# Optimization experiments

Hardware: AMD Instinct MI355X
Metric: run time of the kernel (lower is better)

Reference implementation:

```python
import jax, jax.numpy as jnp
import numpy as np

KS = 2
K = 3 * KS**2 + 3 * KS + 1  # 19 hex-stencil sites
MUL = 16                     # multiplicity of each irrep block
C0 = 0.28209479177387814     # Y_0 integral-normalized, 1/(2*sqrt(pi))
C1 = 0.4886025119029199      # Y_1 coeff, sqrt(3/(4*pi))


def _hex_offsets(ks):
    """Hexagonal stencil offsets in the exact order of spin2coltri2d (center first)."""
    hexagon = [[1, 1], [1, 0], [0, -1], [-1, -1], [-1, 0], [0, 1]]
    offs = [(0, 0)]
    for k in range(1, ks + 1):
        for l in range(6 * k):
            eb = hexagon[l // k]
            ea = hexagon[(l // k + 1) % 6]
            offs.append((eb[0] * (k - l % k) + ea[0] * (l % k),
                         eb[1] * (k - l % k) + ea[1] * (l % k)))
    return offs  # length K


def setup_inputs() -> dict:
    key = jax.random.key(0)
    k1, k2, k3, k4, k5, k6, k7 = jax.random.split(key, 7)
    N, Lx, Ly = 4, 128, 128
    feat = jax.random.normal(k1, (N, Lx, Ly, 4 * MUL), dtype=jnp.float32)
    spin = jax.random.normal(k2, (N, Lx, Ly, 3), dtype=jnp.float32)
    # 'uvw' TensorProduct weights: one (mul_in, mul_out) block per hex position per path
    wshape = (K, MUL, MUL)
    w000 = jax.random.normal(k3, wshape, dtype=jnp.float32)  # 0e x 0e -> 0e
    w011 = jax.random.normal(k4, wshape, dtype=jnp.float32)  # 0e x 1e -> 1e
    w101 = jax.random.normal(k5, wshape, dtype=jnp.float32)  # 1e x 0e -> 1e
    w110 = jax.random.normal(k6, wshape, dtype=jnp.float32)  # 1e x 1e -> 0e (dot)
    w111 = jax.random.normal(k7, wshape, dtype=jnp.float32)  # 1e x 1e -> 1e (cross)
    return {"feat": feat, "spin": spin, "w000": w000, "w011": w011,
            "w101": w101, "w110": w110, "w111": w111}


def reference(feat, spin, w000, w011, w101, w110, w111):
    # --- spin2coltri2d: circular hex-stencil gather via rolls (no pad copy) ---
    offs = _hex_offsets(KS)
    col = jnp.stack([jnp.roll(feat, shift=(-ox, -oy), axis=(1, 2))
                     for (ox, oy) in offs], axis=3)  # (N,Lx,Ly,K,64)
    s = col[..., :MUL]                                       # scalars (N,Lx,Ly,K,16)
    v = col[..., MUL:].reshape(col.shape[:4] + (MUL, 3))     # vectors (N,Lx,Ly,K,16,3)
    # --- spherical harmonics of spin, l=0..1, normalize=False, integral norm ---
    sh1 = C1 * spin[..., jnp.array([1, 2, 0])]               # e3nn l=1 order (y,z,x)
    # --- CG tensor product, path-normalized per output irrep ---
    a_s = 1.0 / np.sqrt(2 * K * MUL)   # two paths feed scalar out
    a_v = 1.0 / np.sqrt(3 * K * MUL)   # three paths feed vector out
    out_s = C0 * jnp.einsum('nxyku,kuw->nxyw', s, w000)
    out_s = out_s + jnp.einsum('nxykui,nxyi,kuw->nxyw', v, sh1, w110) / np.sqrt(3.0)
    out_s = a_s * out_s
    out_v = jnp.einsum('nxyku,nxyi,kuw->nxywi', s, sh1, w011)
    out_v = out_v + C0 * jnp.einsum('nxykui,kuw->nxywi', v, w101)
    cross = jnp.cross(v, sh1[:, :, :, None, None, :])        # 1e x 1e -> 1e
    out_v = out_v + jnp.einsum('nxykui,kuw->nxywi', cross, w111) / np.sqrt(2.0)
    out_v = a_v * out_v
    return jnp.concatenate(
        [out_s, out_v.reshape(out_v.shape[:3] + (3 * MUL,))], axis=-1)
```

## Files before the change

kernel.cpp:

```cpp
#include <hip/hip_runtime.h>

typedef __attribute__((ext_vector_type(8))) short short8;
typedef __attribute__((ext_vector_type(4))) float f32x4;
typedef __attribute__((ext_vector_type(4))) int i32x4;

#define C0F 0.28209479177387814f
#define C1F 0.4886025119029199f
#define IS3 0.5773502691896258f
#define IS2 0.7071067811865476f
#define ASC 0.040555354f
#define AVC 0.033113308f

#define WB 51200
#define FB 30720
#define LDS_TOTAL (WB + FB)

__constant__ int c_doff[20] = {0, 21,20,-1,-21,-20,1,
                               42,41,40,19,-2,-22,-42,-41,-40,-19,2,22, 0};

__device__ inline unsigned short f32_bf16(float x) {
    unsigned int u = __float_as_uint(x);
    return (unsigned short)((u + 0x7FFF + ((u >> 16) & 1)) >> 16);
}

#define GLD16(gp, lp) __builtin_amdgcn_global_load_lds( \
    (const __attribute__((address_space(1))) unsigned int*)(gp), \
    (__attribute__((address_space(3))) unsigned int*)(lp), 16, 0, 0)

__global__ __launch_bounds__(256) void prep_kernel(
    const float* __restrict__ feat,
    const float* __restrict__ w000, const float* __restrict__ w011,
    const float* __restrict__ w101, const float* __restrict__ w110,
    const float* __restrict__ w111, unsigned char* __restrict__ ws)
{
    const int t = threadIdx.x;
    if (blockIdx.x >= 2048) {
        int o = (blockIdx.x - 2048) * 256 + t;
        int m = o / 5120;
        int r1 = o - m * 5120;
        int tap = r1 >> 8;
        int r2 = r1 & 255;
        int w = r2 >> 4;
        int u = r2 & 15;
        const float* W = (m == 0) ? w000 : (m == 1) ? w011 : (m == 2) ? w101 : (m == 3) ? w110 : w111;
        float val = (tap < 19) ? W[tap * 256 + u * 16 + w] : 0.0f;
        ((unsigned short*)ws)[o] = f32_bf16(val);
        return;
    }
    __shared__ float raw[2048];
    const int P0 = blockIdx.x * 32;
    const float4* src = (const float4*)feat + (size_t)P0 * 16;
    float4 l0 = src[t * 2];
    float4 l1 = src[t * 2 + 1];
    *(float4*)&raw[t * 8] = l0;
    *(float4*)&raw[t * 8 + 4] = l1;
    __syncthreads();
    const int p = t >> 3;
    const int c = t & 7;
    const float* r = &raw[p * 64];
    int ch0, stride;
    if (c < 2) { ch0 = c * 8; stride = 1; }
    else { int i = (c - 2) >> 1, uh = (c - 2) & 1; ch0 = 16 + i + 24 * uh; stride = 3; }
    unsigned int pk[4];
#pragma unroll
    for (int e = 0; e < 4; ++e) {
        unsigned int lo = f32_bf16(r[ch0 + stride * (2 * e)]);
        unsigned int hi = f32_bf16(r[ch0 + stride * (2 * e + 1)]);
        pk[e] = lo | (hi << 16);
    }
    const int PX = P0 + p;
    const int gy = PX & 127, gx = (PX >> 7) & 127;
    const int k = (4 * gx + gy + 2) & 7;
    *(i32x4*)(ws + WB + (size_t)PX * 128 + ((c ^ k) << 4)) = *(const i32x4*)pk;
}

__global__ __launch_bounds__(256) void spinconv_mfma(
    const unsigned char* __restrict__ ws, const float* __restrict__ spin,
    float* __restrict__ out)
{
    extern __shared__ char smem[];
    const int tid = threadIdx.x, b = blockIdx.x;
    const int n = b >> 7;
    const int X0 = ((b >> 3) & 15) << 3;
    const int Y0 = (b & 7) << 4;
    const int lane = tid & 63, wv = tid >> 6;
    const int lx = lane & 15;
    const int q = lane >> 4;

    float sp[24];
#pragma unroll
    for (int ti = 0; ti < 2; ++ti)
#pragma unroll
        for (int r = 0; r < 4; ++r) {
            const int x = X0 + 2 * wv + ti;
            const int y = Y0 + (q << 2) + r;
            const int P = (((n << 7) + x) << 7) + y;
            sp[ti * 12 + r * 3 + 0] = spin[3 * P + 0];
            sp[ti * 12 + r * 3 + 1] = spin[3 * P + 1];
            sp[ti * 12 + r * 3 + 2] = spin[3 * P + 2];
        }

    for (int j = 0; j < 13; ++j) {
        const int cid = j * 4 + wv;
        if (cid < 50)
            GLD16(ws + cid * 1024 + lane * 16, smem + cid * 1024);
    }
    const unsigned char* fsrc = ws + WB;
    for (int j = 0; j < 8; ++j) {
        const int cid = j * 4 + wv;
        if (cid < 30) {
            const int sl = cid * 8 + (lane >> 3);
            const int cc = lane & 7;
            const int dx = sl / 20, dy = sl - dx * 20;
            const int gx = (X0 - 2 + dx) & 127;
            const int gy = (Y0 - 2 + dy) & 127;
            GLD16(fsrc + (size_t)((((n << 7) + gx) << 7) + gy) * 128 + cc * 16,
                  smem + WB + cid * 1024);
        }
    }
    __syncthreads();

    const int u0b = (q & 1) << 4;
    const int taph = q >> 1;
    const char* flds = smem + WB;
    const int s0a = (2 * wv + 2) * 20 + lx + 2;
    const int s0b = s0a + 20;

    f32x4 aS0{0,0,0,0}, aS1{0,0,0,0}, aB0{0,0,0,0}, aB1{0,0,0,0}, aB2{0,0,0,0},
          aC0{0,0,0,0}, aC1{0,0,0,0}, aC2{0,0,0,0}, aD0{0,0,0,0}, aD1{0,0,0,0}, aD2{0,0,0,0};
    f32x4 bS0{0,0,0,0}, bS1{0,0,0,0}, bB0{0,0,0,0}, bB1{0,0,0,0}, bB2{0,0,0,0},
          bC0{0,0,0,0}, bC1{0,0,0,0}, bC2{0,0,0,0}, bD0{0,0,0,0}, bD1{0,0,0,0}, bD2{0,0,0,0};

#pragma unroll
    for (int t = 0; t < 10; ++t) {
        const int tap = 2 * t + taph;
        const int d = c_doff[tap];
        const int stA = s0a + d;
        const char* pa = flds + stA * 128;
        const int ka = (stA & 7) << 4;
        short8 xs  = *(const short8*)(pa + ((u0b      ) ^ ka));
        short8 x0  = *(const short8*)(pa + ((u0b + 32) ^ ka));
        short8 x1  = *(const short8*)(pa + ((u0b + 64) ^ ka));
        short8 x2  = *(const short8*)(pa + ((u0b + 96) ^ ka));
        const int stB = s0b + d;
        const char* pb = flds + stB * 128;
        const int kb = (stB & 7) << 4;
        short8 ys  = *(const short8*)(pb + ((u0b      ) ^ kb));
        short8 y0  = *(const short8*)(pb + ((u0b + 32) ^ kb));
        short8 y1  = *(const short8*)(pb + ((u0b + 64) ^ kb));
        short8 y2  = *(const short8*)(pb + ((u0b + 96) ^ kb));
        const char* bb = smem + tap * 512 + lx * 32 + u0b;
        short8 b000 = *(const short8*)(bb);
        short8 b011 = *(const short8*)(bb + 10240);
        short8 b101 = *(const short8*)(bb + 20480);
        short8 b110 = *(const short8*)(bb + 30720);
        short8 b111 = *(const short8*)(bb + 40960);
        aS0 = __builtin_amdgcn_mfma_f32_16x16x32_bf16(xs, b000, aS0, 0, 0, 0);
        aS1 = __builtin_amdgcn_mfma_f32_16x16x32_bf16(xs, b011, aS1, 0, 0, 0);
        aB0 = __builtin_amdgcn_mfma_f32_16x16x32_bf16(x0, b101, aB0, 0, 0, 0);
        aC0 = __builtin_amdgcn_mfma_f32_16x16x32_bf16(x0, b110, aC0, 0, 0, 0);
        aD0 = __builtin_amdgcn_mfma_f32_16x16x32_bf16(x0, b111, aD0, 0, 0, 0);
        aB1 = __builtin_amdgcn_mfma_f32_16x16x32_bf16(x1, b101, aB1, 0, 0, 0);
        aC1 = __builtin_amdgcn_mfma_f32_16x16x32_bf16(x1, b110, aC1, 0, 0, 0);
        aD1 = __builtin_amdgcn_mfma_f32_16x16x32_bf16(x1, b111, aD1, 0, 0, 0);
        aB2 = __builtin_amdgcn_mfma_f32_16x16x32_bf16(x2, b101, aB2, 0, 0, 0);
        aC2 = __builtin_amdgcn_mfma_f32_16x16x32_bf16(x2, b110, aC2, 0, 0, 0);
        aD2 = __builtin_amdgcn_mfma_f32_16x16x32_bf16(x2, b111, aD2, 0, 0, 0);
        bS0 = __builtin_amdgcn_mfma_f32_16x16x32_bf16(ys, b000, bS0, 0, 0, 0);
        bS1 = __builtin_amdgcn_mfma_f32_16x16x32_bf16(ys, b011, bS1, 0, 0, 0);
        bB0 = __builtin_amdgcn_mfma_f32_16x16x32_bf16(y0, b101, bB0, 0, 0, 0);
        bC0 = __builtin_amdgcn_mfma_f32_16x16x32_bf16(y0, b110, bC0, 0, 0, 0);
        bD0 = __builtin_amdgcn_mfma_f32_16x16x32_bf16(y0, b111, bD0, 0, 0, 0);
        bB1 = __builtin_amdgcn_mfma_f32_16x16x32_bf16(y1, b101, bB1, 0, 0, 0);
        bC1 = __builtin_amdgcn_mfma_f32_16x16x32_bf16(y1, b110, bC1, 0, 0, 0);
        bD1 = __builtin_amdgcn_mfma_f32_16x16x32_bf16(y1, b111, bD1, 0, 0, 0);
        bB2 = __builtin_amdgcn_mfma_f32_16x16x32_bf16(y2, b101, bB2, 0, 0, 0);
        bC2 = __builtin_amdgcn_mfma_f32_16x16x32_bf16(y2, b110, bC2, 0, 0, 0);
        bD2 = __builtin_amdgcn_mfma_f32_16x16x32_bf16(y2, b111, bD2, 0, 0, 0);
    }

    const int w = lx;
#pragma unroll
    for (int r = 0; r < 4; ++r) {
        const int y = Y0 + (q << 2) + r;
        {
            const int x = X0 + 2 * wv;
            const int P = (((n << 7) + x) << 7) + y;
            const float s0 = C1F * sp[r * 3 + 1];
            const float s1 = C1F * sp[r * 3 + 2];
            const float s2 = C1F * sp[r * 3 + 0];
            float* o = out + (size_t)P * 64;
            o[w] = ASC * (C0F * aS0[r] + IS3 * (s0 * aC0[r] + s1 * aC1[r] + s2 * aC2[r]));
            o[16 + 3 * w + 0] = AVC * (s0 * aS1[r] + C0F * aB0[r] + IS2 * (s2 * aD1[r] - s1 * aD2[r]));
            o[16 + 3 * w + 1] = AVC * (s1 * aS1[r] + C0F * aB1[r] + IS2 * (s0 * aD2[r] - s2 * aD0[r]));
            o[16 + 3 * w + 2] = AVC * (s2 * aS1[r] + C0F * aB2[r] + IS2 * (s1 * aD0[r] - s0 * aD1[r]));
        }
        {
            const int x = X0 + 2 * wv + 1;
            const int P = (((n << 7) + x) << 7) + y;
            const float s0 = C1F * sp[12 + r * 3 + 1];
            const float s1 = C1F * sp[12 + r * 3 + 2];
            const float s2 = C1F * sp[12 + r * 3 + 0];
            float* o = out + (size_t)P * 64;
            o[w] = ASC * (C0F * bS0[r] + IS3 * (s0 * bC0[r] + s1 * bC1[r] + s2 * bC2[r]));
            o[16 + 3 * w + 0] = AVC * (s0 * bS1[r] + C0F * bB0[r] + IS2 * (s2 * bD1[r] - s1 * bD2[r]));
            o[16 + 3 * w + 1] = AVC * (s1 * bS1[r] + C0F * bB1[r] + IS2 * (s0 * bD2[r] - s2 * bD0[r]));
            o[16 + 3 * w + 2] = AVC * (s2 * bS1[r] + C0F * bB2[r] + IS2 * (s1 * bD0[r] - s0 * bD1[r]));
        }
    }
}

extern "C" void kernel_launch(void* const* d_in, const int* in_sizes, int n_in,
                              void* d_out, int out_size, void* d_ws, size_t ws_size,
                              hipStream_t stream) {
    const float* feat = (const float*)d_in[0];
    const float* spin = (const float*)d_in[1];
    const float* w000 = (const float*)d_in[2];
    const float* w011 = (const float*)d_in[3];
    const float* w101 = (const float*)d_in[4];
    const float* w110 = (const float*)d_in[5];
    const float* w111 = (const float*)d_in[6];
    float* out = (float*)d_out;
    unsigned char* ws = (unsigned char*)d_ws;

    static bool attr_set = false;
    if (!attr_set) {
        (void)hipFuncSetAttribute((const void*)spinconv_mfma,
                                  hipFuncAttributeMaxDynamicSharedMemorySize, LDS_TOTAL);
        attr_set = true;
    }

    hipLaunchKernelGGL(prep_kernel, dim3(2148), dim3(256), 0, stream,
                       feat, w000, w011, w101, w110, w111, ws);
    hipLaunchKernelGGL(spinconv_mfma, dim3(512), dim3(256), LDS_TOTAL, stream,
                       ws, spin, out);
}
```

Before: 90.22 us.

## Fuse feature bf16 conversion into main kernel, drop feature prep pass

The separate prep pass that converted the whole feature map to a swizzled bf16 workspace is removed. The main MFMA kernel now reads fp32 features for its halo tile straight from global memory, converts them to bf16, and scatters them into the swizzled LDS layout with per-element stores. The weight prep shrinks to a 100-block kernel. This removes a full write and re-read of the bf16 feature buffer plus most of the prep launch, at the cost of reading the halo in fp32 (twice the bytes, about 1.56x redundant) and doing many scalar 2-byte LDS stores, which may cause bank conflicts.

```diff
diff --git a/kernel.cpp b/kernel.cpp
--- a/kernel.cpp
+++ b/kernel.cpp
@@ -2,7 +2,6 @@
 
 typedef __attribute__((ext_vector_type(8))) short short8;
 typedef __attribute__((ext_vector_type(4))) float f32x4;
-typedef __attribute__((ext_vector_type(4))) int i32x4;
 
 #define C0F 0.28209479177387814f
 #define C1F 0.4886025119029199f
@@ -27,56 +26,26 @@
     (const __attribute__((address_space(1))) unsigned int*)(gp), \
     (__attribute__((address_space(3))) unsigned int*)(lp), 16, 0, 0)
 
-__global__ __launch_bounds__(256) void prep_kernel(
-    const float* __restrict__ feat,
+__global__ __launch_bounds__(256) void wprep_kernel(
     const float* __restrict__ w000, const float* __restrict__ w011,
     const float* __restrict__ w101, const float* __restrict__ w110,
     const float* __restrict__ w111, unsigned char* __restrict__ ws)
 {
-    const int t = threadIdx.x;
-    if (blockIdx.x >= 2048) {
-        int o = (blockIdx.x - 2048) * 256 + t;
-        int m = o / 5120;
-        int r1 = o - m * 5120;
-        int tap = r1 >> 8;
-        int r2 = r1 & 255;
-        int w = r2 >> 4;
-        int u = r2 & 15;
-        const float* W = (m == 0) ? w000 : (m == 1) ? w011 : (m == 2) ? w101 : (m == 3) ? w110 : w111;
-        float val = (tap < 19) ? W[tap * 256 + u * 16 + w] : 0.0f;
-        ((unsigned short*)ws)[o] = f32_bf16(val);
-        return;
-    }
-    __shared__ float raw[2048];
-    const int P0 = blockIdx.x * 32;
-    const float4* src = (const float4*)feat + (size_t)P0 * 16;
-    float4 l0 = src[t * 2];
-    float4 l1 = src[t * 2 + 1];
-    *(float4*)&raw[t * 8] = l0;
-    *(float4*)&raw[t * 8 + 4] = l1;
-    __syncthreads();
-    const int p = t >> 3;
-    const int c = t & 7;
-    const float* r = &raw[p * 64];
-    int ch0, stride;
-    if (c < 2) { ch0 = c * 8; stride = 1; }
-    else { int i = (c - 2) >> 1, uh = (c - 2) & 1; ch0 = 16 + i + 24 * uh; stride = 3; }
-    unsigned int pk[4];
-#pragma unroll
-    for (int e = 0; e < 4; ++e) {
-        unsigned int lo = f32_bf16(r[ch0 + stride * (2 * e)]);
-        unsigned int hi = f32_bf16(r[ch0 + stride * (2 * e + 1)]);
-        pk[e] = lo | (hi << 16);
-    }
-    const int PX = P0 + p;
-    const int gy = PX & 127, gx = (PX >> 7) & 127;
-    const int k = (4 * gx + gy + 2) & 7;
-    *(i32x4*)(ws + WB + (size_t)PX * 128 + ((c ^ k) << 4)) = *(const i32x4*)pk;
+    int o = blockIdx.x * 256 + threadIdx.x;
+    int m = o / 5120;
+    int r1 = o - m * 5120;
+    int tap = r1 >> 8;
+    int r2 = r1 & 255;
+    int w = r2 >> 4;
+    int u = r2 & 15;
+    const float* W = (m == 0) ? w000 : (m == 1) ? w011 : (m == 2) ? w101 : (m == 3) ? w110 : w111;
+    float val = (tap < 19) ? W[tap * 256 + u * 16 + w] : 0.0f;
+    ((unsigned short*)ws)[o] = f32_bf16(val);
 }
 
 __global__ __launch_bounds__(256) void spinconv_mfma(
-    const unsigned char* __restrict__ ws, const float* __restrict__ spin,
-    float* __restrict__ out)
+    const float* __restrict__ feat, const unsigned char* __restrict__ wbf,
+    const float* __restrict__ spin, float* __restrict__ out)
 {
     extern __shared__ char smem[];
     const int tid = threadIdx.x, b = blockIdx.x;
@@ -103,19 +72,31 @@
     for (int j = 0; j < 13; ++j) {
         const int cid = j * 4 + wv;
         if (cid < 50)
-            GLD16(ws + cid * 1024 + lane * 16, smem + cid * 1024);
-    }
-    const unsigned char* fsrc = ws + WB;
-    for (int j = 0; j < 8; ++j) {
-        const int cid = j * 4 + wv;
-        if (cid < 30) {
-            const int sl = cid * 8 + (lane >> 3);
-            const int cc = lane & 7;
-            const int dx = sl / 20, dy = sl - dx * 20;
-            const int gx = (X0 - 2 + dx) & 127;
-            const int gy = (Y0 - 2 + dy) & 127;
-            GLD16(fsrc + (size_t)((((n << 7) + gx) << 7) + gy) * 128 + cc * 16,
-                  smem + WB + cid * 1024);
+            GLD16(wbf + cid * 1024 + lane * 16, smem + cid * 1024);
+    }
+
+    const int j4 = tid & 15;
+    int dch[4];
+#pragma unroll
+    for (int e = 0; e < 4; ++e) {
+        const int ch = j4 * 4 + e;
+        const int j = ch - 16;
+        dch[e] = (ch < 16) ? ch : (16 + 16 * (j % 3) + j / 3);
+    }
+#pragma unroll
+    for (int r = 0; r < 15; ++r) {
+        const int sl = r * 16 + (tid >> 4);
+        const int dx = sl / 20, dy = sl - dx * 20;
+        const int gx = (X0 - 2 + dx) & 127;
+        const int gy = (Y0 - 2 + dy) & 127;
+        const float4 v = *((const float4*)(feat + (size_t)((((n << 7) + gx) << 7) + gy) * 64) + j4);
+        char* base = smem + WB + sl * 128;
+        const int key = sl & 7;
+        const float vals[4] = {v.x, v.y, v.z, v.w};
+#pragma unroll
+        for (int e = 0; e < 4; ++e) {
+            const int d = dch[e];
+            *(unsigned short*)(base + (((d >> 3) ^ key) << 4) + (d & 7) * 2) = f32_bf16(vals[e]);
         }
     }
     __syncthreads();
@@ -230,8 +211,8 @@
         attr_set = true;
     }
 
-    hipLaunchKernelGGL(prep_kernel, dim3(2148), dim3(256), 0, stream,
-                       feat, w000, w011, w101, w110, w111, ws);
+    hipLaunchKernelGGL(wprep_kernel, dim3(100), dim3(256), 0, stream,
+                       w000, w011, w101, w110, w111, ws);
     hipLaunchKernelGGL(spinconv_mfma, dim3(512), dim3(256), LDS_TOTAL, stream,
-                       ws, spin, out);
-}
+                       feat, ws, spin, out);
+}
```

Measured after the change: 88.72 us. Within noise of the previous version (-1.7%).

## Read stencil features directly from global memory instead of staging halo tile in LDS

Applied to the files above, without the earlier changes.

Drops the LDS staging of the 20x12 halo feature tile and its XOR swizzle. Each lane now loads its tap's bf16 feature vectors straight from global memory (through cache) inside the MFMA loop. LDS now holds only the weights, in a static array, which shrinks per-block LDS and removes the dynamic shared-memory attribute setup. The spin loads also move after the MFMA loop. The cost is global-memory latency inside the unrolled compute loop, plus redundant cache traffic across overlapping taps.

```diff
diff --git a/kernel.cpp b/kernel.cpp
--- a/kernel.cpp
+++ b/kernel.cpp
@@ -12,11 +12,11 @@
 #define AVC 0.033113308f
 
 #define WB 51200
-#define FB 30720
-#define LDS_TOTAL (WB + FB)
-
-__constant__ int c_doff[20] = {0, 21,20,-1,-21,-20,1,
-                               42,41,40,19,-2,-22,-42,-41,-40,-19,2,22, 0};
+
+#define OX0 0
+#define SEL(t_, arr0, arr1) ((taph) ? (arr1) : (arr0))
+
+__constant__ int dummy_unused[1] = {0};
 
 __device__ inline unsigned short f32_bf16(float x) {
     unsigned int u = __float_as_uint(x);
@@ -69,16 +69,14 @@
         pk[e] = lo | (hi << 16);
     }
     const int PX = P0 + p;
-    const int gy = PX & 127, gx = (PX >> 7) & 127;
-    const int k = (4 * gx + gy + 2) & 7;
-    *(i32x4*)(ws + WB + (size_t)PX * 128 + ((c ^ k) << 4)) = *(const i32x4*)pk;
+    *(i32x4*)(ws + WB + (size_t)PX * 128 + (c << 4)) = *(const i32x4*)pk;
 }
 
 __global__ __launch_bounds__(256) void spinconv_mfma(
-    const unsigned char* __restrict__ ws, const float* __restrict__ spin,
-    float* __restrict__ out)
+    const unsigned char* __restrict__ fbf, const unsigned char* __restrict__ wbf,
+    const float* __restrict__ spin, float* __restrict__ out)
 {
-    extern __shared__ char smem[];
+    __shared__ char smem[WB];
     const int tid = threadIdx.x, b = blockIdx.x;
     const int n = b >> 7;
     const int X0 = ((b >> 3) & 15) << 3;
@@ -86,69 +84,46 @@
     const int lane = tid & 63, wv = tid >> 6;
     const int lx = lane & 15;
     const int q = lane >> 4;
-
-    float sp[24];
-#pragma unroll
-    for (int ti = 0; ti < 2; ++ti)
-#pragma unroll
-        for (int r = 0; r < 4; ++r) {
-            const int x = X0 + 2 * wv + ti;
-            const int y = Y0 + (q << 2) + r;
-            const int P = (((n << 7) + x) << 7) + y;
-            sp[ti * 12 + r * 3 + 0] = spin[3 * P + 0];
-            sp[ti * 12 + r * 3 + 1] = spin[3 * P + 1];
-            sp[ti * 12 + r * 3 + 2] = spin[3 * P + 2];
-        }
+    const int u0b = (q & 1) << 4;
+    const int taph = q >> 1;
 
     for (int j = 0; j < 13; ++j) {
         const int cid = j * 4 + wv;
         if (cid < 50)
-            GLD16(ws + cid * 1024 + lane * 16, smem + cid * 1024);
-    }
-    const unsigned char* fsrc = ws + WB;
-    for (int j = 0; j < 8; ++j) {
-        const int cid = j * 4 + wv;
-        if (cid < 30) {
-            const int sl = cid * 8 + (lane >> 3);
-            const int cc = lane & 7;
-            const int dx = sl / 20, dy = sl - dx * 20;
-            const int gx = (X0 - 2 + dx) & 127;
-            const int gy = (Y0 - 2 + dy) & 127;
-            GLD16(fsrc + (size_t)((((n << 7) + gx) << 7) + gy) * 128 + cc * 16,
-                  smem + WB + cid * 1024);
-        }
+            GLD16(wbf + cid * 1024 + lane * 16, smem + cid * 1024);
     }
     __syncthreads();
 
-    const int u0b = (q & 1) << 4;
-    const int taph = q >> 1;
-    const char* flds = smem + WB;
-    const int s0a = (2 * wv + 2) * 20 + lx + 2;
-    const int s0b = s0a + 20;
+    const int xa = X0 + 2 * wv;
+    const int y  = Y0 + lx;
+    const size_t nb = (size_t)n << 14;
 
     f32x4 aS0{0,0,0,0}, aS1{0,0,0,0}, aB0{0,0,0,0}, aB1{0,0,0,0}, aB2{0,0,0,0},
           aC0{0,0,0,0}, aC1{0,0,0,0}, aC2{0,0,0,0}, aD0{0,0,0,0}, aD1{0,0,0,0}, aD2{0,0,0,0};
     f32x4 bS0{0,0,0,0}, bS1{0,0,0,0}, bB0{0,0,0,0}, bB1{0,0,0,0}, bB2{0,0,0,0},
           bC0{0,0,0,0}, bC1{0,0,0,0}, bC2{0,0,0,0}, bD0{0,0,0,0}, bD1{0,0,0,0}, bD2{0,0,0,0};
 
+    constexpr int OXc[20] = {0, 1,1,0,-1,-1,0, 2,2,2,1,0,-1,-2,-2,-2,-1,0,1, 0};
+    constexpr int OYc[20] = {0, 1,0,-1,-1,0,1, 2,1,0,-1,-2,-2,-2,-1,0,1,2,2, 0};
+
 #pragma unroll
     for (int t = 0; t < 10; ++t) {
         const int tap = 2 * t + taph;
-        const int d = c_doff[tap];
-        const int stA = s0a + d;
-        const char* pa = flds + stA * 128;
-        const int ka = (stA & 7) << 4;
-        short8 xs  = *(const short8*)(pa + ((u0b      ) ^ ka));
-        short8 x0  = *(const short8*)(pa + ((u0b + 32) ^ ka));
-        short8 x1  = *(const short8*)(pa + ((u0b + 64) ^ ka));
-        short8 x2  = *(const short8*)(pa + ((u0b + 96) ^ ka));
-        const int stB = s0b + d;
-        const char* pb = flds + stB * 128;
-        const int kb = (stB & 7) << 4;
-        short8 ys  = *(const short8*)(pb + ((u0b      ) ^ kb));
-        short8 y0  = *(const short8*)(pb + ((u0b + 32) ^ kb));
-        short8 y1  = *(const short8*)(pb + ((u0b + 64) ^ kb));
-        short8 y2  = *(const short8*)(pb + ((u0b + 96) ^ kb));
+        const int ox = taph ? OXc[2 * t + 1] : OXc[2 * t];
+        const int oy = taph ? OYc[2 * t + 1] : OYc[2 * t];
+        const int gy  = (y + oy) & 127;
+        const int gxa = (xa + ox) & 127;
+        const int gxb = (xa + 1 + ox) & 127;
+        const unsigned char* pa = fbf + (((nb + (gxa << 7) + gy)) << 7) + u0b;
+        const unsigned char* pb = fbf + (((nb + (gxb << 7) + gy)) << 7) + u0b;
+        short8 xs  = *(const short8*)(pa);
+        short8 x0  = *(const short8*)(pa + 32);
+        short8 x1  = *(const short8*)(pa + 64);
+        short8 x2  = *(const short8*)(pa + 96);
+        short8 ys  = *(const short8*)(pb);
+        short8 y0  = *(const short8*)(pb + 32);
+        short8 y1  = *(const short8*)(pb + 64);
+        short8 y2  = *(const short8*)(pb + 96);
         const char* bb = smem + tap * 512 + lx * 32 + u0b;
         short8 b000 = *(const short8*)(bb);
         short8 b011 = *(const short8*)(bb + 10240);
@@ -179,13 +154,26 @@
         bD2 = __builtin_amdgcn_mfma_f32_16x16x32_bf16(y2, b111, bD2, 0, 0, 0);
     }
 
+    float sp[24];
+#pragma unroll
+    for (int ti = 0; ti < 2; ++ti)
+#pragma unroll
+        for (int r = 0; r < 4; ++r) {
+            const int x = X0 + 2 * wv + ti;
+            const int yy = Y0 + (q << 2) + r;
+            const int P = (((n << 7) + x) << 7) + yy;
+            sp[ti * 12 + r * 3 + 0] = spin[3 * P + 0];
+            sp[ti * 12 + r * 3 + 1] = spin[3 * P + 1];
+            sp[ti * 12 + r * 3 + 2] = spin[3 * P + 2];
+        }
+
     const int w = lx;
 #pragma unroll
     for (int r = 0; r < 4; ++r) {
-        const int y = Y0 + (q << 2) + r;
+        const int yy = Y0 + (q << 2) + r;
         {
             const int x = X0 + 2 * wv;
-            const int P = (((n << 7) + x) << 7) + y;
+            const int P = (((n << 7) + x) << 7) + yy;
             const float s0 = C1F * sp[r * 3 + 1];
             const float s1 = C1F * sp[r * 3 + 2];
             const float s2 = C1F * sp[r * 3 + 0];
@@ -197,7 +185,7 @@
         }
         {
             const int x = X0 + 2 * wv + 1;
-            const int P = (((n << 7) + x) << 7) + y;
+            const int P = (((n << 7) + x) << 7) + yy;
             const float s0 = C1F * sp[12 + r * 3 + 1];
             const float s1 = C1F * sp[12 + r * 3 + 2];
             const float s2 = C1F * sp[12 + r * 3 + 0];
@@ -223,15 +211,8 @@
     float* out = (float*)d_out;
     unsigned char* ws = (unsigned char*)d_ws;
 
-    static bool attr_set = false;
-    if (!attr_set) {
-        (void)hipFuncSetAttribute((const void*)spinconv_mfma,
-                                  hipFuncAttributeMaxDynamicSharedMemorySize, LDS_TOTAL);
-        attr_set = true;
-    }
-
     hipLaunchKernelGGL(prep_kernel, dim3(2148), dim3(256), 0, stream,
                        feat, w000, w011, w101, w110, w111, ws);
-    hipLaunchKernelGGL(spinconv_mfma, dim3(512), dim3(256), LDS_TOTAL, stream,
-                       ws, spin, out);
-}
+    hipLaunchKernelGGL(spinconv_mfma, dim3(512), dim3(256), 0, stream,
+                       ws + WB, ws, spin, out);
+}
```

New measurement: 105.2 us. 1.17x slower.
